# Kernel tuning notes

Measured on AMD Instinct MI355X. Metric: run time of the kernel, lower is better.

## Reference

```python
import jax, jax.numpy as jnp
import numpy as np

KS = 3          # ksize
PAD = 1         # (ksize-1)//2 * dilation, dilation=1

def setup_inputs() -> dict:
    key = jax.random.key(0)
    k1, k2, k3, k4 = jax.random.split(key, 4)
    B, NI, C, H, W = 4, 64, 64, 256, 256
    features = jax.random.normal(k1, (B, NI, H, W), jnp.float32)
    inpt = jax.random.normal(k2, (B, C, H, W), jnp.float32)
    # get_filter: Conv2d(ni, ksize**2, 3, padding=1 reflect, stride=1)
    w = jax.random.normal(k3, (KS * KS, NI, 3, 3), jnp.float32) * 0.05
    b = jax.random.normal(k4, (KS * KS,), jnp.float32) * 0.01
    return {"features": features, "inpt": inpt, "w": w, "b": b}

def reference(features, inpt, w, b):
    # 1) predict per-pixel filters: 3x3 conv with reflect padding
    fpad = jnp.pad(features, ((0, 0), (0, 0), (1, 1), (1, 1)), mode="reflect")
    ff = jax.lax.conv_general_dilated(
        fpad, w, window_strides=(1, 1), padding="VALID",
        dimension_numbers=("NCHW", "OIHW", "NCHW"),
    ) + b[None, :, None, None]                       # [B, 9, H, W]
    ff = jax.nn.softmax(ff, axis=1)                  # softmax over the 9 taps

    # 2) apply per-pixel filter to inpt (shared across channels)
    B, C, H, W = inpt.shape
    ipad = jnp.pad(inpt, ((0, 0), (0, 0), (PAD, PAD), (PAD, PAD)), mode="reflect")
    # unfold: taps in row-major (ki, kj) order, matching torch nn.Unfold
    patches = jnp.stack(
        [ipad[:, :, i:i + H, j:j + W] for i in range(KS) for j in range(KS)],
        axis=2,
    )                                                # [B, C, 9, H, W]
    # out[b,c,h,w] = sum_k patches[b,c,k,h,w] * ff[b,k,h,w]
    return jnp.einsum("bckhw,bkhw->bchw", patches, ff)
```

## Files before the change

### kernel.cpp

```cpp
#include <hip/hip_runtime.h>
#include <math.h>

#define BB 4
#define NI 64
#define CC 64
#define HH 256
#define WW 256
#define HW (HH * WW)

__device__ __forceinline__ int refl(int i, int n) {
    i = (i < 0) ? -i : i;
    return (i >= n) ? (2 * n - 2 - i) : i;
}

__global__ __launch_bounds__(512) void pff_fused2b(
    const float* __restrict__ features,
    const float* __restrict__ inpt,
    const float* __restrict__ wgt,
    const float* __restrict__ bias,
    float* __restrict__ out)
{
    __shared__ float part[2][9][256];

    const int tid  = threadIdx.x;
    const int half = __builtin_amdgcn_readfirstlane(tid >> 8);
    const int p    = tid & 255;
    const int wx = blockIdx.x * 64 + (p & 63);
    const int hy = blockIdx.y * 4 + (p >> 6);
    const int b  = blockIdx.z;

    const int r0 = refl(hy - 1, HH) * WW;
    const int r1 = hy * WW;
    const int r2 = refl(hy + 1, HH) * WW;
    const int iw0 = refl(wx - 1, WW), iw1 = wx, iw2 = refl(wx + 1, WW);

    float acc[9];
    #pragma unroll
    for (int k = 0; k < 9; ++k) acc[k] = 0.f;

    const float* fb = features + (size_t)b * NI * HW + (size_t)half * 32 * HW;
    for (int ni = 0; ni < 32; ++ni) {
        const float* fc = fb + (size_t)ni * HW;
        float f0 = fc[r0 + iw0], f1 = fc[r0 + iw1], f2 = fc[r0 + iw2];
        float f3 = fc[r1 + iw0], f4 = fc[r1 + iw1], f5 = fc[r1 + iw2];
        float f6 = fc[r2 + iw0], f7 = fc[r2 + iw1], f8 = fc[r2 + iw2];
        const float* wn = wgt + (half * 32 + ni) * 9;
        #pragma unroll
        for (int k = 0; k < 9; ++k) {
            const float* wk = wn + k * (NI * 9);
            acc[k] = fmaf(f0, wk[0], acc[k]);
            acc[k] = fmaf(f1, wk[1], acc[k]);
            acc[k] = fmaf(f2, wk[2], acc[k]);
            acc[k] = fmaf(f3, wk[3], acc[k]);
            acc[k] = fmaf(f4, wk[4], acc[k]);
            acc[k] = fmaf(f5, wk[5], acc[k]);
            acc[k] = fmaf(f6, wk[6], acc[k]);
            acc[k] = fmaf(f7, wk[7], acc[k]);
            acc[k] = fmaf(f8, wk[8], acc[k]);
        }
    }

    #pragma unroll
    for (int k = 0; k < 9; ++k) part[half][k][p] = acc[k];
    __syncthreads();
    #pragma unroll
    for (int k = 0; k < 9; ++k)
        acc[k] = part[0][k][p] + part[1][k][p] + bias[k];

    float m = acc[0];
    #pragma unroll
    for (int k = 1; k < 9; ++k) m = fmaxf(m, acc[k]);
    float s = 0.f;
    #pragma unroll
    for (int k = 0; k < 9; ++k) { acc[k] = __expf(acc[k] - m); s += acc[k]; }
    const float inv = 1.f / s;
    #pragma unroll
    for (int k = 0; k < 9; ++k) acc[k] *= inv;

    const float* ib = inpt + (size_t)b * CC * HW + (size_t)half * 32 * HW;
    float* ob       = out  + (size_t)b * CC * HW + (size_t)half * 32 * HW;
    const int opix = r1 + wx;
    for (int c = 0; c < 32; ++c) {
        const float* ic = ib + (size_t)c * HW;
        float o = acc[0] * ic[r0 + iw0];
        o = fmaf(acc[1], ic[r0 + iw1], o);
        o = fmaf(acc[2], ic[r0 + iw2], o);
        o = fmaf(acc[3], ic[r1 + iw0], o);
        o = fmaf(acc[4], ic[r1 + iw1], o);
        o = fmaf(acc[5], ic[r1 + iw2], o);
        o = fmaf(acc[6], ic[r2 + iw0], o);
        o = fmaf(acc[7], ic[r2 + iw1], o);
        o = fmaf(acc[8], ic[r2 + iw2], o);
        ob[(size_t)c * HW + opix] = o;
    }
}

extern "C" void kernel_launch(void* const* d_in, const int* in_sizes, int n_in,
                              void* d_out, int out_size, void* d_ws, size_t ws_size,
                              hipStream_t stream) {
    const float* features = (const float*)d_in[0];
    const float* inpt     = (const float*)d_in[1];
    const float* wgt      = (const float*)d_in[2];
    const float* bias     = (const float*)d_in[3];
    float* out            = (float*)d_out;

    dim3 grid(WW / 64, HH / 4, BB);
    dim3 block(512);
    pff_fused2b<<<grid, block, 0, stream>>>(features, inpt, wgt, bias, out);
}
```

Measured before the change: 79.13 us.

## Compute two output rows per thread and software-prefetch next channel loads

Each thread now handles two vertically adjacent pixels, so it loads a 4x3 window and shares six of those values between the two outputs instead of loading two separate 3x3 windows. Weights are loaded once per pair of pixels, and the grid is halved in the row dimension. Loads for the next channel are issued into a second register set before the current channel is computed, in both the conv and the apply loops. This raises register pressure and halves the block count, which may reduce occupancy and latency hiding.

```diff
diff --git a/kernel.cpp b/kernel.cpp
--- a/kernel.cpp
+++ b/kernel.cpp
@@ -13,7 +13,7 @@
     return (i >= n) ? (2 * n - 2 - i) : i;
 }
 
-__global__ __launch_bounds__(512) void pff_fused2b(
+__global__ __launch_bounds__(512) void pff_fused2c(
     const float* __restrict__ features,
     const float* __restrict__ inpt,
     const float* __restrict__ wgt,
@@ -25,73 +25,129 @@
     const int tid  = threadIdx.x;
     const int half = __builtin_amdgcn_readfirstlane(tid >> 8);
     const int p    = tid & 255;
-    const int wx = blockIdx.x * 64 + (p & 63);
-    const int hy = blockIdx.y * 4 + (p >> 6);
-    const int b  = blockIdx.z;
+    const int wx  = blockIdx.x * 64 + (p & 63);
+    const int tr  = p >> 6;
+    const int hy0 = blockIdx.y * 8 + tr * 2;
+    const int b   = blockIdx.z;
 
-    const int r0 = refl(hy - 1, HH) * WW;
-    const int r1 = hy * WW;
-    const int r2 = refl(hy + 1, HH) * WW;
+    const int ra = refl(hy0 - 1, HH) * WW;
+    const int rb = hy0 * WW;
+    const int rc = (hy0 + 1) * WW;
+    const int rd = refl(hy0 + 2, HH) * WW;
     const int iw0 = refl(wx - 1, WW), iw1 = wx, iw2 = refl(wx + 1, WW);
 
-    float acc[9];
+    int off[12];
+    off[0] = ra + iw0; off[1]  = ra + iw1; off[2]  = ra + iw2;
+    off[3] = rb + iw0; off[4]  = rb + iw1; off[5]  = rb + iw2;
+    off[6] = rc + iw0; off[7]  = rc + iw1; off[8]  = rc + iw2;
+    off[9] = rd + iw0; off[10] = rd + iw1; off[11] = rd + iw2;
+
+    float accA[9], accB[9];
     #pragma unroll
-    for (int k = 0; k < 9; ++k) acc[k] = 0.f;
+    for (int k = 0; k < 9; ++k) { accA[k] = 0.f; accB[k] = 0.f; }
 
     const float* fb = features + (size_t)b * NI * HW + (size_t)half * 32 * HW;
+    float f[12], g[12];
+    #pragma unroll
+    for (int t = 0; t < 12; ++t) f[t] = fb[off[t]];
+
     for (int ni = 0; ni < 32; ++ni) {
-        const float* fc = fb + (size_t)ni * HW;
-        float f0 = fc[r0 + iw0], f1 = fc[r0 + iw1], f2 = fc[r0 + iw2];
-        float f3 = fc[r1 + iw0], f4 = fc[r1 + iw1], f5 = fc[r1 + iw2];
-        float f6 = fc[r2 + iw0], f7 = fc[r2 + iw1], f8 = fc[r2 + iw2];
+        if (ni < 31) {
+            const float* fn = fb + (size_t)(ni + 1) * HW;
+            #pragma unroll
+            for (int t = 0; t < 12; ++t) g[t] = fn[off[t]];
+        }
         const float* wn = wgt + (half * 32 + ni) * 9;
         #pragma unroll
         for (int k = 0; k < 9; ++k) {
             const float* wk = wn + k * (NI * 9);
-            acc[k] = fmaf(f0, wk[0], acc[k]);
-            acc[k] = fmaf(f1, wk[1], acc[k]);
-            acc[k] = fmaf(f2, wk[2], acc[k]);
-            acc[k] = fmaf(f3, wk[3], acc[k]);
-            acc[k] = fmaf(f4, wk[4], acc[k]);
-            acc[k] = fmaf(f5, wk[5], acc[k]);
-            acc[k] = fmaf(f6, wk[6], acc[k]);
-            acc[k] = fmaf(f7, wk[7], acc[k]);
-            acc[k] = fmaf(f8, wk[8], acc[k]);
+            const float w0 = wk[0], w1 = wk[1], w2 = wk[2];
+            const float w3 = wk[3], w4 = wk[4], w5 = wk[5];
+            const float w6 = wk[6], w7 = wk[7], w8 = wk[8];
+            accA[k] = fmaf(f[0], w0, accA[k]);
+            accB[k] = fmaf(f[3], w0, accB[k]);
+            accA[k] = fmaf(f[1], w1, accA[k]);
+            accB[k] = fmaf(f[4], w1, accB[k]);
+            accA[k] = fmaf(f[2], w2, accA[k]);
+            accB[k] = fmaf(f[5], w2, accB[k]);
+            accA[k] = fmaf(f[3], w3, accA[k]);
+            accB[k] = fmaf(f[6], w3, accB[k]);
+            accA[k] = fmaf(f[4], w4, accA[k]);
+            accB[k] = fmaf(f[7], w4, accB[k]);
+            accA[k] = fmaf(f[5], w5, accA[k]);
+            accB[k] = fmaf(f[8], w5, accB[k]);
+            accA[k] = fmaf(f[6], w6, accA[k]);
+            accB[k] = fmaf(f[9], w6, accB[k]);
+            accA[k] = fmaf(f[7], w7, accA[k]);
+            accB[k] = fmaf(f[10], w7, accB[k]);
+            accA[k] = fmaf(f[8], w8, accA[k]);
+            accB[k] = fmaf(f[11], w8, accB[k]);
         }
+        #pragma unroll
+        for (int t = 0; t < 12; ++t) f[t] = g[t];
     }
 
     #pragma unroll
-    for (int k = 0; k < 9; ++k) part[half][k][p] = acc[k];
+    for (int k = 0; k < 9; ++k) part[half][k][p] = accA[k];
     __syncthreads();
     #pragma unroll
-    for (int k = 0; k < 9; ++k)
-        acc[k] = part[0][k][p] + part[1][k][p] + bias[k];
+    for (int k = 0; k < 9; ++k) accA[k] = part[0][k][p] + part[1][k][p] + bias[k];
+    __syncthreads();
+    #pragma unroll
+    for (int k = 0; k < 9; ++k) part[half][k][p] = accB[k];
+    __syncthreads();
+    #pragma unroll
+    for (int k = 0; k < 9; ++k) accB[k] = part[0][k][p] + part[1][k][p] + bias[k];
 
-    float m = acc[0];
-    #pragma unroll
-    for (int k = 1; k < 9; ++k) m = fmaxf(m, acc[k]);
-    float s = 0.f;
-    #pragma unroll
-    for (int k = 0; k < 9; ++k) { acc[k] = __expf(acc[k] - m); s += acc[k]; }
-    const float inv = 1.f / s;
-    #pragma unroll
-    for (int k = 0; k < 9; ++k) acc[k] *= inv;
+    {
+        float m = accA[0];
+        #pragma unroll
+        for (int k = 1; k < 9; ++k) m = fmaxf(m, accA[k]);
+        float s = 0.f;
+        #pragma unroll
+        for (int k = 0; k < 9; ++k) { accA[k] = __expf(accA[k] - m); s += accA[k]; }
+        const float inv = 1.f / s;
+        #pragma unroll
+        for (int k = 0; k < 9; ++k) accA[k] *= inv;
+    }
+    {
+        float m = accB[0];
+        #pragma unroll
+        for (int k = 1; k < 9; ++k) m = fmaxf(m, accB[k]);
+        float s = 0.f;
+        #pragma unroll
+        for (int k = 0; k < 9; ++k) { accB[k] = __expf(accB[k] - m); s += accB[k]; }
+        const float inv = 1.f / s;
+        #pragma unroll
+        for (int k = 0; k < 9; ++k) accB[k] *= inv;
+    }
 
     const float* ib = inpt + (size_t)b * CC * HW + (size_t)half * 32 * HW;
     float* ob       = out  + (size_t)b * CC * HW + (size_t)half * 32 * HW;
-    const int opix = r1 + wx;
+    const int oA = rb + wx, oB = rc + wx;
+
+    #pragma unroll
+    for (int t = 0; t < 12; ++t) f[t] = ib[off[t]];
     for (int c = 0; c < 32; ++c) {
-        const float* ic = ib + (size_t)c * HW;
-        float o = acc[0] * ic[r0 + iw0];
-        o = fmaf(acc[1], ic[r0 + iw1], o);
-        o = fmaf(acc[2], ic[r0 + iw2], o);
-        o = fmaf(acc[3], ic[r1 + iw0], o);
-        o = fmaf(acc[4], ic[r1 + iw1], o);
-        o = fmaf(acc[5], ic[r1 + iw2], o);
-        o = fmaf(acc[6], ic[r2 + iw0], o);
-        o = fmaf(acc[7], ic[r2 + iw1], o);
-        o = fmaf(acc[8], ic[r2 + iw2], o);
-        ob[(size_t)c * HW + opix] = o;
+        if (c < 31) {
+            const float* in2 = ib + (size_t)(c + 1) * HW;
+            #pragma unroll
+            for (int t = 0; t < 12; ++t) g[t] = in2[off[t]];
+        }
+        float vA = accA[0] * f[0];
+        float vB = accB[0] * f[3];
+        vA = fmaf(accA[1], f[1],  vA);  vB = fmaf(accB[1], f[4],  vB);
+        vA = fmaf(accA[2], f[2],  vA);  vB = fmaf(accB[2], f[5],  vB);
+        vA = fmaf(accA[3], f[3],  vA);  vB = fmaf(accB[3], f[6],  vB);
+        vA = fmaf(accA[4], f[4],  vA);  vB = fmaf(accB[4], f[7],  vB);
+        vA = fmaf(accA[5], f[5],  vA);  vB = fmaf(accB[5], f[8],  vB);
+        vA = fmaf(accA[6], f[6],  vA);  vB = fmaf(accB[6], f[9],  vB);
+        vA = fmaf(accA[7], f[7],  vA);  vB = fmaf(accB[7], f[10], vB);
+        vA = fmaf(accA[8], f[8],  vA);  vB = fmaf(accB[8], f[11], vB);
+        ob[(size_t)c * HW + oA] = vA;
+        ob[(size_t)c * HW + oB] = vB;
+        #pragma unroll
+        for (int t = 0; t < 12; ++t) f[t] = g[t];
     }
 }
 
@@ -104,7 +160,7 @@
     const float* bias     = (const float*)d_in[3];
     float* out            = (float*)d_out;
 
-    dim3 grid(WW / 64, HH / 4, BB);
+    dim3 grid(WW / 64, HH / 8, BB);
     dim3 block(512);
-    pff_fused2b<<<grid, block, 0, stream>>>(features, inpt, wgt, bias, out);
+    pff_fused2c<<<grid, block, 0, stream>>>(features, inpt, wgt, bias, out);
 }
```

After: 97.55 us. 1.23x slower.
